# Performance work log

Measured on AMD Instinct MI355X. Metric: run time of the kernel, lower is better.

## Reference

```python
import jax, jax.numpy as jnp
import numpy as np

EMBED_DIM = 1024
N, L = 4, 4096


def setup_inputs() -> dict:
    key = jax.random.key(0)
    ks = jax.random.split(key, 9)
    s = 1.0 / np.sqrt(EMBED_DIM)
    return {
        "q": jax.random.normal(ks[0], (N, L, EMBED_DIM), jnp.float32),
        "k": jax.random.normal(ks[1], (N, L, EMBED_DIM), jnp.float32),
        "v": jax.random.normal(ks[2], (N, L, EMBED_DIM), jnp.float32),
        "Wq": jax.random.normal(ks[3], (EMBED_DIM, EMBED_DIM), jnp.float32) * s,
        "bq": jax.random.normal(ks[4], (EMBED_DIM,), jnp.float32) * s,
        "Wk": jax.random.normal(ks[5], (EMBED_DIM, EMBED_DIM), jnp.float32) * s,
        "bk": jax.random.normal(ks[6], (EMBED_DIM,), jnp.float32) * s,
        "Wv": jax.random.normal(ks[7], (EMBED_DIM, EMBED_DIM), jnp.float32) * s,
        "bv": jax.random.normal(ks[8], (EMBED_DIM,), jnp.float32) * s,
    }


def reference(q, k, v, Wq, bq, Wk, bk, Wv, bv):
    scale = 1.0 / (q.shape[-1] ** 0.5)  # 1/sqrt(embed_dim), single-head
    pq = jnp.einsum("nle,fe->nlf", q, Wq) + bq  # (N, L, E)
    pk = jnp.einsum("nle,fe->nlf", k, Wk) + bk
    pv = jnp.einsum("nle,fe->nlf", v, Wv) + bv
    scores = jnp.einsum("nle,nme->nlm", pq, pk) * scale  # (N, L, L)
    attn = jax.nn.softmax(scores, axis=-1)
    return jnp.einsum("nlm,nme->nle", attn, pv)  # (N, L, E)
```

## Files before the change

### kernel.cpp

```cpp
#include <hip/hip_runtime.h>

typedef unsigned short u16;
typedef __bf16  bf16x8 __attribute__((ext_vector_type(8)));
typedef float   f32x4  __attribute__((ext_vector_type(4)));
typedef unsigned short us8 __attribute__((ext_vector_type(8)));
typedef _Float16 f16x8 __attribute__((ext_vector_type(8)));
typedef float   fl4   __attribute__((ext_vector_type(4)));

#define AS1 __attribute__((address_space(1)))
#define AS3 __attribute__((address_space(3)))

__device__ __forceinline__ u16 f2bf(float f) {
    union { float f; unsigned u; } x; x.f = f;
    unsigned r = x.u + 0x7fffu + ((x.u >> 16) & 1u);
    return (u16)(r >> 16);
}

__global__ __launch_bounds__(256) void cvt3_f32_bf16(const float* __restrict__ in0,
                                                     const float* __restrict__ in1,
                                                     const float* __restrict__ in2,
                                                     u16* __restrict__ out0,
                                                     u16* __restrict__ out1,
                                                     u16* __restrict__ out2, int n8) {
    const float* in = blockIdx.y == 0 ? in0 : (blockIdx.y == 1 ? in1 : in2);
    u16* out        = blockIdx.y == 0 ? out0 : (blockIdx.y == 1 ? out1 : out2);
    int i = blockIdx.x * blockDim.x + threadIdx.x;
    int stride = gridDim.x * blockDim.x;
    for (; i < n8; i += stride) {
        const fl4* p = (const fl4*)(in + (long)i * 8);
        fl4 a = p[0], b = p[1];
        us8 o;
#pragma unroll
        for (int j = 0; j < 4; ++j) { o[j] = f2bf(a[j]); o[4 + j] = f2bf(b[j]); }
        *(us8*)(out + (long)i * 8) = o;
    }
}

template <int MODE>
__global__ __launch_bounds__(512, 2) void gemm256d(const u16* __restrict__ A,
                                                   const u16* __restrict__ B,
                                                   void* __restrict__ Cout,
                                                   const float* __restrict__ bias,
                                                   float scale, int K,
                                                   int lda, int ldb, int ldc,
                                                   long sAz, long sBz, long sCz) {
    __shared__ alignas(16) char lds8[2 * 65536];

    const int t    = threadIdx.x;
    const int lane = t & 63;
    const int wid  = t >> 6;
    const int wr   = wid >> 2;
    const int wc   = wid & 3;
    const int fr   = lane & 15;
    const int kq   = lane >> 4;

    const int gx  = gridDim.x;
    const int nwg = gx * gridDim.y;
    const int wg  = blockIdx.y * gx + blockIdx.x;
    const int swz = (wg & 7) * (nwg >> 3) + (wg >> 3);
    const long brow = (long)(swz / gx) * 256;
    const long bcol = (long)(swz % gx) * 256;

    const u16* Az = A + sAz * blockIdx.z;
    const u16* Bz = B + sBz * blockIdx.z;

    const int trow = t >> 3;
    const int tc8  = ((t & 7) ^ (trow & 7)) * 8;
    long offA[4], offB[4];
#pragma unroll
    for (int r = 0; r < 4; ++r) offA[r] = (brow + r * 64 + trow) * (long)lda + tc8;
#pragma unroll
    for (int r = 0; r < 4; ++r) offB[r] = (bcol + r * 64 + trow) * (long)ldb + tc8;

    int aRow[8], bRow[4], aCh[2];
#pragma unroll
    for (int m = 0; m < 8; ++m) aRow[m] = (wr * 128 + m * 16 + fr) * 128;
#pragma unroll
    for (int n = 0; n < 4; ++n) bRow[n] = 32768 + (wc * 64 + n * 16 + fr) * 128;
#pragma unroll
    for (int ks = 0; ks < 2; ++ks) aCh[ks] = (((ks << 2) | kq) ^ (fr & 7)) * 16;

    const int NT = K >> 6;
    f32x4 acc[8][4] = {};

    {
        char* bb0 = lds8;
#pragma unroll
        for (int r = 0; r < 4; ++r)
            __builtin_amdgcn_global_load_lds((const AS1 unsigned*)(Az + offA[r]),
                                             (AS3 unsigned*)(bb0 + r * 8192 + t * 16), 16, 0, 0);
#pragma unroll
        for (int r = 0; r < 4; ++r)
            __builtin_amdgcn_global_load_lds((const AS1 unsigned*)(Bz + offB[r]),
                                             (AS3 unsigned*)(bb0 + 32768 + r * 8192 + t * 16), 16, 0, 0);
    }
    __syncthreads();

    int cur = 0;
    for (int T = 0; T < NT; ++T) {
        char* bb  = lds8 + cur * 65536;
        char* bbn = lds8 + (cur ^ 1) * 65536;

        if (T + 1 < NT) {
            const long kcol = (long)(T + 1) << 6;
#pragma unroll
            for (int r = 0; r < 4; ++r)
                __builtin_amdgcn_global_load_lds((const AS1 unsigned*)(Az + offA[r] + kcol),
                                                 (AS3 unsigned*)(bbn + r * 8192 + t * 16), 16, 0, 0);
#pragma unroll
            for (int r = 0; r < 4; ++r)
                __builtin_amdgcn_global_load_lds((const AS1 unsigned*)(Bz + offB[r] + kcol),
                                                 (AS3 unsigned*)(bbn + 32768 + r * 8192 + t * 16), 16, 0, 0);
        }

        bf16x8 bfv[2][4], afl[2][4], afh[2][4];
#pragma unroll
        for (int ks = 0; ks < 2; ++ks)
#pragma unroll
            for (int n = 0; n < 4; ++n)
                bfv[ks][n] = *(const bf16x8*)(bb + bRow[n] + aCh[ks]);
#pragma unroll
        for (int ks = 0; ks < 2; ++ks)
#pragma unroll
            for (int m = 0; m < 4; ++m)
                afl[ks][m] = *(const bf16x8*)(bb + aRow[m] + aCh[ks]);

        __builtin_amdgcn_s_setprio(1);
#pragma unroll
        for (int ks = 0; ks < 2; ++ks)
#pragma unroll
            for (int m = 0; m < 4; ++m)
#pragma unroll
                for (int n = 0; n < 4; ++n)
                    acc[m][n] = __builtin_amdgcn_mfma_f32_16x16x32_bf16(afl[ks][m], bfv[ks][n], acc[m][n], 0, 0, 0);
        __builtin_amdgcn_s_setprio(0);

#pragma unroll
        for (int ks = 0; ks < 2; ++ks)
#pragma unroll
            for (int m = 0; m < 4; ++m)
                afh[ks][m] = *(const bf16x8*)(bb + aRow[4 + m] + aCh[ks]);

        __builtin_amdgcn_s_setprio(1);
#pragma unroll
        for (int ks = 0; ks < 2; ++ks)
#pragma unroll
            for (int m = 0; m < 4; ++m)
#pragma unroll
                for (int n = 0; n < 4; ++n)
                    acc[4 + m][n] = __builtin_amdgcn_mfma_f32_16x16x32_bf16(afh[ks][m], bfv[ks][n], acc[4 + m][n], 0, 0, 0);
        __builtin_amdgcn_s_setprio(0);

        __syncthreads();
        cur ^= 1;
    }

    const long crow = brow + wr * 128;
    const long ccol = bcol + wc * 64;
    const long cz = sCz * blockIdx.z;
#pragma unroll
    for (int m = 0; m < 8; ++m) {
#pragma unroll
        for (int n = 0; n < 4; ++n) {
#pragma unroll
            for (int j = 0; j < 4; ++j) {
                long r = crow + m * 16 + kq * 4 + j;
                long c = ccol + n * 16 + fr;
                float vv = acc[m][n][j];
                if (MODE == 0)      { vv += bias[c]; ((u16*)Cout)[cz + r * ldc + c] = f2bf(vv); }
                else if (MODE == 1) { vv += bias[r]; ((u16*)Cout)[cz + r * ldc + c] = f2bf(vv); }
                else if (MODE == 2) { ((_Float16*)Cout)[cz + r * ldc + c] = (_Float16)(vv * scale); }
                else                { ((float*)Cout)[cz + r * ldc + c] = vv; }
            }
        }
    }
}

template <int MODE>
__global__ __launch_bounds__(256, 2) void gemm128(const u16* __restrict__ A,
                                                  const u16* __restrict__ B,
                                                  void* __restrict__ Cout,
                                                  const float* __restrict__ bias,
                                                  float scale, int K,
                                                  int lda, int ldb, int ldc,
                                                  long sAz, long sBz, long sCz) {
    __shared__ alignas(16) char lds8[2 * 32768];

    const int t    = threadIdx.x;
    const int lane = t & 63;
    const int wid  = t >> 6;
    const int wr   = wid >> 1;
    const int wc   = wid & 1;
    const int fr   = lane & 15;
    const int kq   = lane >> 4;

    const int gx  = gridDim.x;
    const int nwg = gx * gridDim.y;
    const int wg  = blockIdx.y * gx + blockIdx.x;
    const int swz = (wg & 7) * (nwg >> 3) + (wg >> 3);
    const long brow = (long)(swz / gx) * 128;
    const long bcol = (long)(swz % gx) * 128;

    const u16* Az = A + sAz * blockIdx.z;
    const u16* Bz = B + sBz * blockIdx.z;

    const int trow = t >> 3;
    const int tc8  = ((t & 7) ^ (trow & 7)) * 8;
    long offA[4], offB[4];
#pragma unroll
    for (int r = 0; r < 4; ++r) offA[r] = (brow + r * 32 + trow) * (long)lda + tc8;
#pragma unroll
    for (int r = 0; r < 4; ++r) offB[r] = (bcol + r * 32 + trow) * (long)ldb + tc8;

    int aRow[4], bRow[4], aCh[2];
#pragma unroll
    for (int m = 0; m < 4; ++m) aRow[m] = (wr * 64 + m * 16 + fr) * 128;
#pragma unroll
    for (int n = 0; n < 4; ++n) bRow[n] = 16384 + (wc * 64 + n * 16 + fr) * 128;
#pragma unroll
    for (int ks = 0; ks < 2; ++ks) aCh[ks] = (((ks << 2) | kq) ^ (fr & 7)) * 16;

    const int NT = K >> 6;
    f32x4 acc[4][4] = {};

    {
        char* bb0 = lds8;
#pragma unroll
        for (int r = 0; r < 4; ++r)
            __builtin_amdgcn_global_load_lds((const AS1 unsigned*)(Az + offA[r]),
                                             (AS3 unsigned*)(bb0 + r * 4096 + t * 16), 16, 0, 0);
#pragma unroll
        for (int r = 0; r < 4; ++r)
            __builtin_amdgcn_global_load_lds((const AS1 unsigned*)(Bz + offB[r]),
                                             (AS3 unsigned*)(bb0 + 16384 + r * 4096 + t * 16), 16, 0, 0);
    }
    __syncthreads();

    int cur = 0;
    for (int T = 0; T < NT; ++T) {
        char* bb  = lds8 + cur * 32768;
        char* bbn = lds8 + (cur ^ 1) * 32768;

        if (T + 1 < NT) {
            const long kcol = (long)(T + 1) << 6;
#pragma unroll
            for (int r = 0; r < 4; ++r)
                __builtin_amdgcn_global_load_lds((const AS1 unsigned*)(Az + offA[r] + kcol),
                                                 (AS3 unsigned*)(bbn + r * 4096 + t * 16), 16, 0, 0);
#pragma unroll
            for (int r = 0; r < 4; ++r)
                __builtin_amdgcn_global_load_lds((const AS1 unsigned*)(Bz + offB[r] + kcol),
                                                 (AS3 unsigned*)(bbn + 16384 + r * 4096 + t * 16), 16, 0, 0);
        }

        bf16x8 af[2][4], bfv[2][4];
#pragma unroll
        for (int ks = 0; ks < 2; ++ks)
#pragma unroll
            for (int m = 0; m < 4; ++m)
                af[ks][m] = *(const bf16x8*)(bb + aRow[m] + aCh[ks]);
#pragma unroll
        for (int ks = 0; ks < 2; ++ks)
#pragma unroll
            for (int n = 0; n < 4; ++n)
                bfv[ks][n] = *(const bf16x8*)(bb + bRow[n] + aCh[ks]);

        __builtin_amdgcn_s_setprio(1);
#pragma unroll
        for (int ks = 0; ks < 2; ++ks)
#pragma unroll
            for (int m = 0; m < 4; ++m)
#pragma unroll
                for (int n = 0; n < 4; ++n)
                    acc[m][n] = __builtin_amdgcn_mfma_f32_16x16x32_bf16(af[ks][m], bfv[ks][n], acc[m][n], 0, 0, 0);
        __builtin_amdgcn_s_setprio(0);

        __syncthreads();
        cur ^= 1;
    }

    const long crow = brow + wr * 64;
    const long ccol = bcol + wc * 64;
    const long cz = sCz * blockIdx.z;
#pragma unroll
    for (int m = 0; m < 4; ++m) {
#pragma unroll
        for (int n = 0; n < 4; ++n) {
#pragma unroll
            for (int j = 0; j < 4; ++j) {
                long r = crow + m * 16 + kq * 4 + j;
                long c = ccol + n * 16 + fr;
                float vv = acc[m][n][j];
                if (MODE == 0)      { vv += bias[c]; ((u16*)Cout)[cz + r * ldc + c] = f2bf(vv); }
                else if (MODE == 1) { vv += bias[r]; ((u16*)Cout)[cz + r * ldc + c] = f2bf(vv); }
                else if (MODE == 2) { ((_Float16*)Cout)[cz + r * ldc + c] = (_Float16)(vv * scale); }
                else                { ((float*)Cout)[cz + r * ldc + c] = vv; }
            }
        }
    }
}

__global__ __launch_bounds__(256) void softmax_row(u16* __restrict__ S, int L) {
    const long row = blockIdx.x;
    u16* rp = S + row * L;
    const int t = threadIdx.x;
    const int lane = t & 63, wid = t >> 6;

    f16x8 h0 = *(const f16x8*)(rp + t * 16);
    f16x8 h1 = *(const f16x8*)(rp + t * 16 + 8);
    float x[16];
#pragma unroll
    for (int j = 0; j < 8; ++j) { x[j] = (float)h0[j]; x[8 + j] = (float)h1[j]; }

    float m = -1e30f;
#pragma unroll
    for (int j = 0; j < 16; ++j) m = fmaxf(m, x[j]);
#pragma unroll
    for (int o = 32; o; o >>= 1) m = fmaxf(m, __shfl_xor(m, o));

    __shared__ float redmax[4], redsum[4];
    if (lane == 0) redmax[wid] = m;
    __syncthreads();
    m = fmaxf(fmaxf(redmax[0], redmax[1]), fmaxf(redmax[2], redmax[3]));

    float e[16], s = 0.f;
#pragma unroll
    for (int j = 0; j < 16; ++j) { e[j] = __expf(x[j] - m); s += e[j]; }
#pragma unroll
    for (int o = 32; o; o >>= 1) s += __shfl_xor(s, o);
    if (lane == 0) redsum[wid] = s;
    __syncthreads();
    s = redsum[0] + redsum[1] + redsum[2] + redsum[3];
    float inv = 1.f / s;

    us8 o0, o1;
#pragma unroll
    for (int j = 0; j < 8; ++j) { o0[j] = f2bf(e[j] * inv); o1[j] = f2bf(e[8 + j] * inv); }
    *(us8*)(rp + t * 16) = o0;
    *(us8*)(rp + t * 16 + 8) = o1;
}

extern "C" void kernel_launch(void* const* d_in, const int* in_sizes, int n_in,
                              void* d_out, int out_size, void* d_ws, size_t ws_size,
                              hipStream_t stream) {
    (void)in_sizes; (void)n_in; (void)out_size;
    const float* q  = (const float*)d_in[0];
    const float* k  = (const float*)d_in[1];
    const float* v  = (const float*)d_in[2];
    const float* Wq = (const float*)d_in[3];
    const float* bq = (const float*)d_in[4];
    const float* Wk = (const float*)d_in[5];
    const float* bk = (const float*)d_in[6];
    const float* Wv = (const float*)d_in[7];
    const float* bv = (const float*)d_in[8];
    float* out = (float*)d_out;

    constexpr long MB = 1l << 20;
    char* ws = (char*)d_ws;
    u16* pq  = (u16*)(ws + 0 * MB);
    u16* pk  = (u16*)(ws + 32 * MB);
    u16* pvT = (u16*)(ws + 64 * MB);
    u16* Wqb = (u16*)(ws + 96 * MB);
    u16* Wkb = (u16*)(ws + 98 * MB);
    u16* Wvb = (u16*)(ws + 100 * MB);
    u16* qb  = (u16*)(ws + 104 * MB);
    u16* kb  = (u16*)(ws + 136 * MB);
    u16* vb  = (u16*)(ws + 168 * MB);
    u16* S4  = (u16*)(ws + 104 * MB);

    const int L = 4096, E = 1024, NB = 4;
    const int n8_x = (NB * L * E) / 8;
    const int n8_w = (E * E) / 8;
    const bool z4 = ws_size >= (size_t)233 * MB;

    cvt3_f32_bf16<<<dim3(1024, 3), 256, 0, stream>>>(q, k, v, qb, kb, vb, n8_x);
    cvt3_f32_bf16<<<dim3(256, 3), 256, 0, stream>>>(Wq, Wk, Wv, Wqb, Wkb, Wvb, n8_w);

    dim3 gproj(4, 64, 1);
    gemm256d<0><<<gproj, 512, 0, stream>>>(qb, Wqb, pq, bq, 1.f, E, E, E, E, 0, 0, 0);
    gemm256d<0><<<gproj, 512, 0, stream>>>(kb, Wkb, pk, bk, 1.f, E, E, E, E, 0, 0, 0);
    dim3 gpv(64, 4, 1);
    gemm256d<1><<<gpv, 512, 0, stream>>>(Wvb, vb, pvT, bv, 1.f, E, E, E, NB * L, 0, 0, 0);

    const float scale = 0.03125f;
    if (z4) {
        gemm256d<2><<<dim3(16, 16, 4), 512, 0, stream>>>(pq, pk, (void*)S4,
                                                         nullptr, scale, E, E, E, L,
                                                         (long)L * E, (long)L * E, (long)L * L);
        softmax_row<<<NB * L, 256, 0, stream>>>(S4, L);
        gemm256d<3><<<dim3(4, 16, 4), 512, 0, stream>>>(S4, pvT, out,
                                                        nullptr, 1.f, L, L, NB * L, E,
                                                        (long)L * L, (long)L, (long)L * E);
    } else {
        u16* S2 = S4;
        for (int p = 0; p < 2; ++p) {
            const long zb = p * 2;
            gemm256d<2><<<dim3(16, 16, 2), 512, 0, stream>>>(pq + zb * L * E, pk + zb * L * E, (void*)S2,
                                                             nullptr, scale, E, E, E, L,
                                                             (long)L * E, (long)L * E, (long)L * L);
            softmax_row<<<2 * L, 256, 0, stream>>>(S2, L);
            gemm128<3><<<dim3(8, 32, 2), 256, 0, stream>>>(S2, pvT + zb * L, out + zb * L * E,
                                                           nullptr, 1.f, L, L, NB * L, E,
                                                           (long)L * L, (long)L, (long)L * E);
        }
    }
}
```

Baseline: 451.0 us.

## Merge conversion launches, drop MFMA setprio, use 256-tile GEMM in fallback

Merges the two f32-to-bf16 conversion launches into one six-slice launch, which saves a kernel launch. Removes the s_setprio raise and lower around the MFMA blocks in both GEMM kernels. In the small-workspace fallback path, swaps the 128-tile PV GEMM for the 256-tile kernel. The priority change may alter how waves interleave memory and matrix work, and the weight slices now launch 1024 blocks of mostly idle threads.

```diff
diff --git a/kernel.cpp b/kernel.cpp
--- a/kernel.cpp
+++ b/kernel.cpp
@@ -16,14 +16,26 @@
     return (u16)(r >> 16);
 }
 
-__global__ __launch_bounds__(256) void cvt3_f32_bf16(const float* __restrict__ in0,
-                                                     const float* __restrict__ in1,
-                                                     const float* __restrict__ in2,
-                                                     u16* __restrict__ out0,
-                                                     u16* __restrict__ out1,
-                                                     u16* __restrict__ out2, int n8) {
-    const float* in = blockIdx.y == 0 ? in0 : (blockIdx.y == 1 ? in1 : in2);
-    u16* out        = blockIdx.y == 0 ? out0 : (blockIdx.y == 1 ? out1 : out2);
+__global__ __launch_bounds__(256) void cvt6(const float* __restrict__ q,
+                                            const float* __restrict__ k,
+                                            const float* __restrict__ v,
+                                            const float* __restrict__ Wq,
+                                            const float* __restrict__ Wk,
+                                            const float* __restrict__ Wv,
+                                            u16* __restrict__ qb, u16* __restrict__ kb,
+                                            u16* __restrict__ vb, u16* __restrict__ Wqb,
+                                            u16* __restrict__ Wkb, u16* __restrict__ Wvb,
+                                            int n8x, int n8w) {
+    const int y = blockIdx.y;
+    const float* in; u16* out; int n8;
+    switch (y) {
+        case 0: in = q;  out = qb;  n8 = n8x; break;
+        case 1: in = k;  out = kb;  n8 = n8x; break;
+        case 2: in = v;  out = vb;  n8 = n8x; break;
+        case 3: in = Wq; out = Wqb; n8 = n8w; break;
+        case 4: in = Wk; out = Wkb; n8 = n8w; break;
+        default: in = Wv; out = Wvb; n8 = n8w; break;
+    }
     int i = blockIdx.x * blockDim.x + threadIdx.x;
     int stride = gridDim.x * blockDim.x;
     for (; i < n8; i += stride) {
@@ -125,7 +137,6 @@
             for (int m = 0; m < 4; ++m)
                 afl[ks][m] = *(const bf16x8*)(bb + aRow[m] + aCh[ks]);
 
-        __builtin_amdgcn_s_setprio(1);
 #pragma unroll
         for (int ks = 0; ks < 2; ++ks)
 #pragma unroll
@@ -133,7 +144,6 @@
 #pragma unroll
                 for (int n = 0; n < 4; ++n)
                     acc[m][n] = __builtin_amdgcn_mfma_f32_16x16x32_bf16(afl[ks][m], bfv[ks][n], acc[m][n], 0, 0, 0);
-        __builtin_amdgcn_s_setprio(0);
 
 #pragma unroll
         for (int ks = 0; ks < 2; ++ks)
@@ -141,7 +151,6 @@
             for (int m = 0; m < 4; ++m)
                 afh[ks][m] = *(const bf16x8*)(bb + aRow[4 + m] + aCh[ks]);
 
-        __builtin_amdgcn_s_setprio(1);
 #pragma unroll
         for (int ks = 0; ks < 2; ++ks)
 #pragma unroll
@@ -149,7 +158,6 @@
 #pragma unroll
                 for (int n = 0; n < 4; ++n)
                     acc[4 + m][n] = __builtin_amdgcn_mfma_f32_16x16x32_bf16(afh[ks][m], bfv[ks][n], acc[4 + m][n], 0, 0, 0);
-        __builtin_amdgcn_s_setprio(0);
 
         __syncthreads();
         cur ^= 1;
@@ -265,7 +273,6 @@
             for (int n = 0; n < 4; ++n)
                 bfv[ks][n] = *(const bf16x8*)(bb + bRow[n] + aCh[ks]);
 
-        __builtin_amdgcn_s_setprio(1);
 #pragma unroll
         for (int ks = 0; ks < 2; ++ks)
 #pragma unroll
@@ -273,7 +280,6 @@
 #pragma unroll
                 for (int n = 0; n < 4; ++n)
                     acc[m][n] = __builtin_amdgcn_mfma_f32_16x16x32_bf16(af[ks][m], bfv[ks][n], acc[m][n], 0, 0, 0);
-        __builtin_amdgcn_s_setprio(0);
 
         __syncthreads();
         cur ^= 1;
@@ -373,8 +379,8 @@
     const int n8_w = (E * E) / 8;
     const bool z4 = ws_size >= (size_t)233 * MB;
 
-    cvt3_f32_bf16<<<dim3(1024, 3), 256, 0, stream>>>(q, k, v, qb, kb, vb, n8_x);
-    cvt3_f32_bf16<<<dim3(256, 3), 256, 0, stream>>>(Wq, Wk, Wv, Wqb, Wkb, Wvb, n8_w);
+    cvt6<<<dim3(1024, 6), 256, 0, stream>>>(q, k, v, Wq, Wk, Wv,
+                                            qb, kb, vb, Wqb, Wkb, Wvb, n8_x, n8_w);
 
     dim3 gproj(4, 64, 1);
     gemm256d<0><<<gproj, 512, 0, stream>>>(qb, Wqb, pq, bq, 1.f, E, E, E, E, 0, 0, 0);
@@ -384,8 +390,7 @@
 
     const float scale = 0.03125f;
     if (z4) {
-        gemm256d<2><<<dim3(16, 16, 4), 512, 0, stream>>>(pq, pk, (void*)S4,
-                                                         nullptr, scale, E, E, E, L,
+        gemm256d<2><<<dim3(16, 16, 4), 512, 0, stream>>>(pq, pk, S4, nullptr, scale, E, E, E, L,
                                                          (long)L * E, (long)L * E, (long)L * L);
         softmax_row<<<NB * L, 256, 0, stream>>>(S4, L);
         gemm256d<3><<<dim3(4, 16, 4), 512, 0, stream>>>(S4, pvT, out,
@@ -395,13 +400,13 @@
         u16* S2 = S4;
         for (int p = 0; p < 2; ++p) {
             const long zb = p * 2;
-            gemm256d<2><<<dim3(16, 16, 2), 512, 0, stream>>>(pq + zb * L * E, pk + zb * L * E, (void*)S2,
-                                                             nullptr, scale, E, E, E, L,
+            gemm256d<2><<<dim3(16, 16, 2), 512, 0, stream>>>(pq + zb * L * E, pk + zb * L * E,
+                                                             S2, nullptr, scale, E, E, E, L,
                                                              (long)L * E, (long)L * E, (long)L * L);
             softmax_row<<<2 * L, 256, 0, stream>>>(S2, L);
-            gemm128<3><<<dim3(8, 32, 2), 256, 0, stream>>>(S2, pvT + zb * L, out + zb * L * E,
-                                                           nullptr, 1.f, L, L, NB * L, E,
-                                                           (long)L * L, (long)L, (long)L * E);
+            gemm256d<3><<<dim3(4, 16, 2), 512, 0, stream>>>(S2, pvT + zb * L, out + zb * L * E,
+                                                            nullptr, 1.f, L, L, NB * L, E,
+                                                            (long)L * L, (long)L, (long)L * E);
         }
     }
 }
```

New measurement: 443.9 us. No clear change (-1.6%).
